# Kernel optimization log

Measured on AMD Instinct MI355X. Metric: run time of the kernel, lower is better.

The kernel has to match this reference:

```python
import jax, jax.numpy as jnp
import numpy as np

IN_C = 512
OUT_C = 1024
N = 8192


def _xavier(key, shape):
    fan_in, fan_out = shape[1], shape[0]
    limit = float(np.sqrt(6.0 / (fan_in + fan_out)))
    return jax.random.uniform(key, shape, jnp.float32, -limit, limit)


def setup_inputs() -> dict:
    key = jax.random.key(0)
    ks = jax.random.split(key, 20)
    inp = {
        'x': jax.random.normal(ks[0], (IN_C, N), jnp.float32),
        'c_prev_dim0': jax.random.normal(ks[1], (OUT_C, N), jnp.float32),
        'h_prev_dim0': jax.random.normal(ks[2], (OUT_C, N), jnp.float32),
        'c_prev_dim1': jax.random.normal(ks[3], (OUT_C, N), jnp.float32),
        'h_prev_dim1': jax.random.normal(ks[4], (OUT_C, N), jnp.float32),
    }
    names_x = ['w_ii', 'w_if', 'w_ig', 'w_io']
    names_h = ['w_hi', 'w_hf', 'w_hg', 'w_ho']
    names_b = ['b_i', 'b_f', 'b_g', 'b_o']
    k = 5
    for n in names_x:
        inp[n] = _xavier(ks[k], (OUT_C, IN_C)); k += 1
    for n in names_h:
        inp[n] = _xavier(ks[k], (OUT_C, OUT_C)); k += 1
    for n in names_b:
        inp[n] = _xavier(ks[k], (OUT_C, 1)); k += 1
    inp['weighted_sum'] = jax.random.uniform(ks[k], (2,), jnp.float32)
    return inp


def reference(x, c_prev_dim0, h_prev_dim0, c_prev_dim1, h_prev_dim1,
              w_ii, w_if, w_ig, w_io,
              w_hi, w_hf, w_hg, w_ho,
              b_i, b_f, b_g, b_o,
              weighted_sum):
    # Input projections shared by both spatial directions: (out, N)
    xi = w_ii @ x
    xf = w_if @ x
    xg = w_ig @ x
    xo = w_io @ x

    def gates(h_prev, c_prev):
        i = jax.nn.sigmoid(xi + w_hi @ h_prev + b_i)
        f = jax.nn.sigmoid(xf + w_hf @ h_prev + b_f)
        g = jnp.tanh(xg + w_hg @ h_prev + b_g)
        o = jax.nn.sigmoid(xo + w_ho @ h_prev + b_o)
        c = f * c_prev + i * g
        h = o * jnp.tanh(c)
        return c, h

    ct0, ht0 = gates(h_prev_dim0, c_prev_dim0)
    ct1, ht1 = gates(h_prev_dim1, c_prev_dim1)
    ct = ct0 * weighted_sum[0] + ct1 * weighted_sum[1]
    ht = ht0 * weighted_sum[0] + ht1 * weighted_sum[1]
    return ct, ht
```

## Files before the change

kernel.cpp:

```cpp
#include <hip/hip_runtime.h>
#include <cstdint>
#include <cstddef>

#define IN_C  512
#define OUT_C 1024
#define NSAMP 8192
#define KTOT  1536

typedef __bf16 bf16x8 __attribute__((ext_vector_type(8)));
typedef float  f32x4  __attribute__((ext_vector_type(4)));

#define SBAR()   __builtin_amdgcn_s_barrier()
#define SFENCE() __builtin_amdgcn_sched_barrier(0)
#define VM0()    asm volatile("s_waitcnt vmcnt(0)")

__device__ __forceinline__ unsigned short f2bf(float f) {
    unsigned int u = __float_as_uint(f);
    u += 0x7FFFu + ((u >> 16) & 1u);
    return (unsigned short)(u >> 16);
}
__device__ __forceinline__ float sigmoid_f(float x) { return 1.0f / (1.0f + __expf(-x)); }
__device__ __forceinline__ float tanh_f(float x) {
    float e = __expf(2.0f * x);
    return 1.0f - 2.0f / (e + 1.0f);
}

__global__ void tcvt_kernel(const float* __restrict__ in, unsigned short* __restrict__ out,
                            int R, int C) {
    __shared__ float t[32][33];
    const int tx = threadIdx.x, ty = threadIdx.y;
    const int c0 = blockIdx.x * 32, r0 = blockIdx.y * 32;
#pragma unroll
    for (int i = 0; i < 4; ++i)
        t[ty + i * 8][tx] = in[(size_t)(r0 + ty + i * 8) * C + (c0 + tx)];
    __syncthreads();
#pragma unroll
    for (int i = 0; i < 4; ++i)
        out[(size_t)(c0 + ty + i * 8) * R + (r0 + tx)] = f2bf(t[tx][ty + i * 8]);
}

__global__ void packA_kernel(const float* __restrict__ x0, const float* __restrict__ x1,
                             const float* __restrict__ x2, const float* __restrict__ x3,
                             const float* __restrict__ h0, const float* __restrict__ h1,
                             const float* __restrict__ h2, const float* __restrict__ h3,
                             unsigned short* __restrict__ Ap) {
    const int idx = blockIdx.x * 256 + threadIdx.x;
    const int m = idx / 192, k8 = idx % 192;
    const int g = m & 3, r = m >> 2;
    const float* src;
    if (k8 < 64) {
        const float* a = (g & 2) ? ((g & 1) ? x3 : x2) : ((g & 1) ? x1 : x0);
        src = a + (size_t)r * IN_C + k8 * 8;
    } else {
        const float* a = (g & 2) ? ((g & 1) ? h3 : h2) : ((g & 1) ? h1 : h0);
        src = a + (size_t)r * OUT_C + (k8 - 64) * 8;
    }
    float4 v0 = reinterpret_cast<const float4*>(src)[0];
    float4 v1 = reinterpret_cast<const float4*>(src)[1];
    ushort4 o0, o1;
    o0.x = f2bf(v0.x); o0.y = f2bf(v0.y); o0.z = f2bf(v0.z); o0.w = f2bf(v0.w);
    o1.x = f2bf(v1.x); o1.y = f2bf(v1.y); o1.z = f2bf(v1.z); o1.w = f2bf(v1.w);
    ushort4* dst = reinterpret_cast<ushort4*>(Ap + (size_t)m * KTOT + k8 * 8);
    dst[0] = o0; dst[1] = o1;
}

__global__ __launch_bounds__(512, 2) void mdlstm_main(
    const unsigned short* __restrict__ Ap,
    const unsigned short* __restrict__ xT,
    const unsigned short* __restrict__ h0T,
    const unsigned short* __restrict__ h1T,
    const float* __restrict__ b_i, const float* __restrict__ b_f,
    const float* __restrict__ b_g, const float* __restrict__ b_o,
    const float* __restrict__ cp0, const float* __restrict__ cp1,
    const float* __restrict__ wsum,
    float* __restrict__ out)
{
    __shared__ __align__(16) unsigned char smem[131072];

    const int tid  = threadIdx.x;
    const int lane = tid & 63;
    const int wid  = tid >> 6;
    const int wm   = wid >> 2;
    const int wn   = wid & 3;
    const int g4   = lane >> 4;
    const int l16  = lane & 15;

    const int by    = blockIdx.y;
    const int bcol  = blockIdx.x * 128;
    const int browM = by * 256;

    f32x4 acc[8][4];
#pragma unroll
    for (int mf = 0; mf < 8; ++mf)
#pragma unroll
        for (int nf = 0; nf < 4; ++nf)
            acc[mf][nf] = (f32x4){0.f, 0.f, 0.f, 0.f};

    auto stage_A = [&](int P, int hA, int j1) {
#pragma unroll
        for (int c = 0; c < 2; ++c) {
            const int u    = c * 8192 + tid * 16;
            const int rloc = (u >> 6) & 127;
            const int kb   = (u & 63) ^ (((u >> 7) & 3) << 4);
            const char* src = (const char*)Ap
                + ((size_t)(browM + hA * 128 + rloc) * KTOT + j1 * 64 + c * 32) * 2 + kb;
            __builtin_amdgcn_global_load_lds((const unsigned int*)src,
                (unsigned int*)(smem + P * 65536 + hA * 16384 + u), 16, 0, 0);
        }
    };
    auto stage_B = [&](int P, int d, int j2) {
#pragma unroll
        for (int c = 0; c < 2; ++c) {
            const int u    = c * 8192 + tid * 16;
            const int rloc = (u >> 6) & 127;
            const int kb   = (u & 63) ^ (((u >> 7) & 3) << 4);
            const char* src;
            if (j2 < 8) {
                src = (const char*)xT + ((size_t)(bcol + rloc) * IN_C + j2 * 64 + c * 32) * 2 + kb;
            } else {
                const unsigned short* hsrc = d ? h1T : h0T;
                src = (const char*)hsrc + ((size_t)(bcol + rloc) * OUT_C + (j2 - 8) * 64 + c * 32) * 2 + kb;
            }
            __builtin_amdgcn_global_load_lds((const unsigned int*)src,
                (unsigned int*)(smem + P * 65536 + 32768 + d * 16384 + u), 16, 0, 0);
        }
    };

    auto swzb = [](int u) { return u ^ (((u >> 7) & 3) << 4); };
    auto fragA = [&](int P, int mf, int kk) -> bf16x8 {
        const int u = kk * 8192 + (mf * 16 + l16) * 64 + g4 * 16;
        return *reinterpret_cast<const bf16x8*>(smem + P * 65536 + wm * 16384 + swzb(u));
    };
    auto fragB = [&](int P, int nf, int kk) -> bf16x8 {
        const int u = kk * 8192 + ((wn & 1) * 64 + nf * 16 + l16) * 64 + g4 * 16;
        return *reinterpret_cast<const bf16x8*>(smem + P * 65536 + 32768 + (wn >> 1) * 16384 + swzb(u));
    };

    bf16x8 aF[2][2];
    bf16x8 bF[4][2];

    auto cluster = [&](int M) {
        __builtin_amdgcn_s_setprio(1);
#pragma unroll
        for (int kk = 0; kk < 2; ++kk)
#pragma unroll
            for (int mi = 0; mi < 2; ++mi)
#pragma unroll
                for (int nf = 0; nf < 4; ++nf)
                    acc[M + mi][nf] = __builtin_amdgcn_mfma_f32_16x16x32_bf16(
                        aF[mi][kk], bF[nf][kk], acc[M + mi][nf], 0, 0, 0);
        __builtin_amdgcn_s_setprio(0);
    };
    auto loadA = [&](int P, int mf) {
#pragma unroll
        for (int kk = 0; kk < 2; ++kk) { aF[0][kk] = fragA(P, mf, kk); aF[1][kk] = fragA(P, mf + 1, kk); }
    };
    auto loadB = [&](int P) {
#pragma unroll
        for (int nf = 0; nf < 4; ++nf)
#pragma unroll
            for (int kk = 0; kk < 2; ++kk) bF[nf][kk] = fragB(P, nf, kk);
    };

    auto ktile = [&](int j, int P, int PN) {
        const bool st = (j < 23);
        loadB(P);
        loadA(P, 0);
        cluster(0);
        loadA(P, 2);
        if (st) { stage_A(PN, 0, j + 1); stage_A(PN, 1, j + 1); }
        cluster(2);
        loadA(P, 4);
        if (st) { stage_B(PN, 0, j + 1); stage_B(PN, 1, j + 1); }
        cluster(4);
        loadA(P, 6);
        cluster(6);
        SFENCE(); VM0(); SFENCE();
        SBAR();
    };

    stage_A(0, 0, 0); stage_A(0, 1, 0);
    stage_B(0, 0, 0); stage_B(0, 1, 0);
    SFENCE(); VM0(); SFENCE();
    SBAR();

#pragma unroll 1
    for (int jj = 0; jj < 12; ++jj) {
        ktile(2 * jj,     0, 1);
        ktile(2 * jj + 1, 1, 0);
    }

    const float w0 = wsum[0], w1 = wsum[1];
    const int   d  = wn >> 1;
    const float* cp = d ? cp1 : cp0;
    const float wd  = d ? w1 : w0;

    float rc[8][4], rh[8][4];
#pragma unroll
    for (int mf = 0; mf < 8; ++mf) {
        const int orow = by * 64 + wm * 32 + mf * 4 + g4;
        const float bi = b_i[orow], bff = b_f[orow], bg = b_g[orow], bo = b_o[orow];
#pragma unroll
        for (int nf = 0; nf < 4; ++nf) {
            const int scol = bcol + (wn & 1) * 64 + nf * 16 + l16;
            float i_ = sigmoid_f(acc[mf][nf][0] + bi);
            float f_ = sigmoid_f(acc[mf][nf][1] + bff);
            float g_ = tanh_f  (acc[mf][nf][2] + bg);
            float o_ = sigmoid_f(acc[mf][nf][3] + bo);
            float cc = f_ * cp[(size_t)orow * NSAMP + scol] + i_ * g_;
            float hh = o_ * tanh_f(cc);
            rc[mf][nf] = wd * cc;
            rh[mf][nf] = wd * hh;
        }
    }

    float* ex = (float*)smem;
    const int rbase = (wm * 2 + (wn & 1)) * 4096;
    if (d == 1) {
#pragma unroll
        for (int mf = 0; mf < 8; ++mf)
#pragma unroll
            for (int nf = 0; nf < 4; ++nf) {
                const int slot = rbase + (mf * 4 + nf) * 64 + lane;
                ex[slot]        = rc[mf][nf];
                ex[slot + 2048] = rh[mf][nf];
            }
    }
    SBAR();
    if (d == 0) {
#pragma unroll
        for (int mf = 0; mf < 8; ++mf) {
            const int orow = by * 64 + wm * 32 + mf * 4 + g4;
#pragma unroll
            for (int nf = 0; nf < 4; ++nf) {
                const int scol = bcol + (wn & 1) * 64 + nf * 16 + l16;
                const int slot = rbase + (mf * 4 + nf) * 64 + lane;
                out[(size_t)orow * NSAMP + scol] = rc[mf][nf] + ex[slot];
                out[(size_t)OUT_C * NSAMP + (size_t)orow * NSAMP + scol] = rh[mf][nf] + ex[slot + 2048];
            }
        }
    }
}

extern "C" void kernel_launch(void* const* d_in, const int* in_sizes, int n_in,
                              void* d_out, int out_size, void* d_ws, size_t ws_size,
                              hipStream_t stream) {
    (void)in_sizes; (void)n_in; (void)out_size; (void)ws_size;

    const float* x    = (const float*)d_in[0];
    const float* cp0  = (const float*)d_in[1];
    const float* hp0  = (const float*)d_in[2];
    const float* cp1  = (const float*)d_in[3];
    const float* hp1  = (const float*)d_in[4];
    const float* b_i  = (const float*)d_in[13];
    const float* b_f  = (const float*)d_in[14];
    const float* b_g  = (const float*)d_in[15];
    const float* b_o  = (const float*)d_in[16];
    const float* wsum = (const float*)d_in[17];
    float* out = (float*)d_out;

    char* ws = (char*)d_ws;
    unsigned short* xT  = (unsigned short*)(ws);
    unsigned short* h0T = (unsigned short*)(ws + (size_t)8  * 1024 * 1024);
    unsigned short* h1T = (unsigned short*)(ws + (size_t)24 * 1024 * 1024);
    unsigned short* Ap  = (unsigned short*)(ws + (size_t)40 * 1024 * 1024);

    dim3 tb(32, 8);
    tcvt_kernel<<<dim3(NSAMP / 32, IN_C  / 32), tb, 0, stream>>>(x,   xT,  IN_C,  NSAMP);
    tcvt_kernel<<<dim3(NSAMP / 32, OUT_C / 32), tb, 0, stream>>>(hp0, h0T, OUT_C, NSAMP);
    tcvt_kernel<<<dim3(NSAMP / 32, OUT_C / 32), tb, 0, stream>>>(hp1, h1T, OUT_C, NSAMP);

    packA_kernel<<<(4096 * 192) / 256, 256, 0, stream>>>(
        (const float*)d_in[5], (const float*)d_in[6], (const float*)d_in[7], (const float*)d_in[8],
        (const float*)d_in[9], (const float*)d_in[10], (const float*)d_in[11], (const float*)d_in[12],
        Ap);

    mdlstm_main<<<dim3(NSAMP / 128, OUT_C / 64), 512, 0, stream>>>(
        Ap, xT, h0T, h1T, b_i, b_f, b_g, b_o, cp0, cp1, wsum, out);
}
```

Measured before the change: 238.0 us.

## Precompute staging source pointers, relayout LDS tiles, fully unroll k-loop

```diff
diff --git a/kernel.cpp b/kernel.cpp
--- a/kernel.cpp
+++ b/kernel.cpp
@@ -96,44 +96,56 @@
         for (int nf = 0; nf < 4; ++nf)
             acc[mf][nf] = (f32x4){0.f, 0.f, 0.f, 0.f};
 
-    auto stage_A = [&](int P, int hA, int j1) {
-#pragma unroll
-        for (int c = 0; c < 2; ++c) {
-            const int u    = c * 8192 + tid * 16;
-            const int rloc = (u >> 6) & 127;
-            const int kb   = (u & 63) ^ (((u >> 7) & 3) << 4);
-            const char* src = (const char*)Ap
-                + ((size_t)(browM + hA * 128 + rloc) * KTOT + j1 * 64 + c * 32) * 2 + kb;
-            __builtin_amdgcn_global_load_lds((const unsigned int*)src,
-                (unsigned int*)(smem + P * 65536 + hA * 16384 + u), 16, 0, 0);
-        }
+    const int swzlo = (g4 * 16) ^ (((l16 >> 1) & 3) << 4);
+    unsigned char* const aBase = smem + wm * 8192 + l16 * 64 + swzlo;
+    unsigned char* const bBase = smem + 65536 + (wn >> 1) * 32768 + (wn & 1) * 4096
+                                 + l16 * 64 + swzlo;
+
+    const int srow = tid >> 2;
+    const int skb  = (tid * 16) & 63;
+
+    const char* srcA0; const char* srcA1; const char* srcA2; const char* srcA3;
+    {
+        auto mk = [&](int c) -> const char* {
+            const int row = (c & 1) * 128 + srow;
+            const int kk  = c >> 1;
+            return (const char*)Ap + ((size_t)(browM + row) * KTOT + kk * 32) * 2
+                   + (skb ^ (((row >> 1) & 3) << 4));
+        };
+        srcA0 = mk(0); srcA1 = mk(1); srcA2 = mk(2); srcA3 = mk(3);
+    }
+    const int swB = ((srow >> 1) & 3) << 4;
+    const char* srcBx0 = (const char*)xT  + ((size_t)(bcol + srow) * IN_C)  * 2 + (skb ^ swB);
+    const char* srcBx1 = srcBx0 + 64;
+    const char* srcBh00 = (const char*)h0T + ((size_t)(bcol + srow) * OUT_C) * 2 + (skb ^ swB);
+    const char* srcBh01 = srcBh00 + 64;
+    const char* srcBh10 = (const char*)h1T + ((size_t)(bcol + srow) * OUT_C) * 2 + (skb ^ swB);
+    const char* srcBh11 = srcBh10 + 64;
+
+    auto stage_A = [&](int P, int j) {
+        __builtin_amdgcn_global_load_lds((const unsigned int*)(srcA0 + j * 128),
+            (unsigned int*)(smem + P * 32768 +     0 + tid * 16), 16, 0, 0);
+        __builtin_amdgcn_global_load_lds((const unsigned int*)(srcA1 + j * 128),
+            (unsigned int*)(smem + P * 32768 +  8192 + tid * 16), 16, 0, 0);
+        __builtin_amdgcn_global_load_lds((const unsigned int*)(srcA2 + j * 128),
+            (unsigned int*)(smem + P * 32768 + 16384 + tid * 16), 16, 0, 0);
+        __builtin_amdgcn_global_load_lds((const unsigned int*)(srcA3 + j * 128),
+            (unsigned int*)(smem + P * 32768 + 24576 + tid * 16), 16, 0, 0);
     };
     auto stage_B = [&](int P, int d, int j2) {
-#pragma unroll
-        for (int c = 0; c < 2; ++c) {
-            const int u    = c * 8192 + tid * 16;
-            const int rloc = (u >> 6) & 127;
-            const int kb   = (u & 63) ^ (((u >> 7) & 3) << 4);
-            const char* src;
-            if (j2 < 8) {
-                src = (const char*)xT + ((size_t)(bcol + rloc) * IN_C + j2 * 64 + c * 32) * 2 + kb;
-            } else {
-                const unsigned short* hsrc = d ? h1T : h0T;
-                src = (const char*)hsrc + ((size_t)(bcol + rloc) * OUT_C + (j2 - 8) * 64 + c * 32) * 2 + kb;
-            }
-            __builtin_amdgcn_global_load_lds((const unsigned int*)src,
-                (unsigned int*)(smem + P * 65536 + 32768 + d * 16384 + u), 16, 0, 0);
-        }
-    };
-
-    auto swzb = [](int u) { return u ^ (((u >> 7) & 3) << 4); };
+        const char* s0 = (j2 < 8) ? (srcBx0 + j2 * 128) : ((d ? srcBh10 : srcBh00) + (j2 - 8) * 128);
+        const char* s1 = (j2 < 8) ? (srcBx1 + j2 * 128) : ((d ? srcBh11 : srcBh01) + (j2 - 8) * 128);
+        __builtin_amdgcn_global_load_lds((const unsigned int*)s0,
+            (unsigned int*)(smem + 65536 + d * 32768 + P * 16384 +    0 + tid * 16), 16, 0, 0);
+        __builtin_amdgcn_global_load_lds((const unsigned int*)s1,
+            (unsigned int*)(smem + 65536 + d * 32768 + P * 16384 + 8192 + tid * 16), 16, 0, 0);
+    };
+
     auto fragA = [&](int P, int mf, int kk) -> bf16x8 {
-        const int u = kk * 8192 + (mf * 16 + l16) * 64 + g4 * 16;
-        return *reinterpret_cast<const bf16x8*>(smem + P * 65536 + wm * 16384 + swzb(u));
+        return *reinterpret_cast<const bf16x8*>(aBase + P * 32768 + kk * 16384 + mf * 1024);
     };
     auto fragB = [&](int P, int nf, int kk) -> bf16x8 {
-        const int u = kk * 8192 + ((wn & 1) * 64 + nf * 16 + l16) * 64 + g4 * 16;
-        return *reinterpret_cast<const bf16x8*>(smem + P * 65536 + 32768 + (wn >> 1) * 16384 + swzb(u));
+        return *reinterpret_cast<const bf16x8*>(bBase + P * 16384 + kk * 8192 + nf * 1024);
     };
 
     bf16x8 aF[2][2];
@@ -162,13 +174,20 @@
             for (int kk = 0; kk < 2; ++kk) bF[nf][kk] = fragB(P, nf, kk);
     };
 
-    auto ktile = [&](int j, int P, int PN) {
+    stage_A(0, 0);
+    stage_B(0, 0, 0); stage_B(0, 1, 0);
+    SFENCE(); VM0(); SFENCE();
+    SBAR();
+
+#pragma unroll
+    for (int j = 0; j < 24; ++j) {
+        const int P = j & 1, PN = P ^ 1;
         const bool st = (j < 23);
         loadB(P);
         loadA(P, 0);
         cluster(0);
         loadA(P, 2);
-        if (st) { stage_A(PN, 0, j + 1); stage_A(PN, 1, j + 1); }
+        if (st) stage_A(PN, j + 1);
         cluster(2);
         loadA(P, 4);
         if (st) { stage_B(PN, 0, j + 1); stage_B(PN, 1, j + 1); }
@@ -177,17 +196,6 @@
         cluster(6);
         SFENCE(); VM0(); SFENCE();
         SBAR();
-    };
-
-    stage_A(0, 0, 0); stage_A(0, 1, 0);
-    stage_B(0, 0, 0); stage_B(0, 1, 0);
-    SFENCE(); VM0(); SFENCE();
-    SBAR();
-
-#pragma unroll 1
-    for (int jj = 0; jj < 12; ++jj) {
-        ktile(2 * jj,     0, 1);
-        ktile(2 * jj + 1, 1, 0);
     }
 
     const float w0 = wsum[0], w1 = wsum[1];
```

New measurement: 236.5 us. No clear change (-0.6%).
